# Kernel tuning notes

Measured on AMD Instinct MI355X. Metric: run time of the kernel, lower is better.

Reference implementation:

```python
import jax, jax.numpy as jnp
import numpy as np


def setup_inputs() -> dict:
    key = jax.random.key(0)
    ks = jax.random.split(key, 5)
    B, S, D = 2, 2048, 1024
    scale = 0.02
    return {
        "x": jax.random.normal(ks[0], (B, S, D), dtype=jnp.float32),
        "q_proj_weight": jax.random.normal(ks[1], (D, D), dtype=jnp.float32) * scale,
        "k_proj_weight": jax.random.normal(ks[2], (D, D), dtype=jnp.float32) * scale,
        "v_proj_weight": jax.random.normal(ks[3], (D, D), dtype=jnp.float32) * scale,
        "o_proj_weight": jax.random.normal(ks[4], (D, D), dtype=jnp.float32) * scale,
    }


def reference(x, q_proj_weight, k_proj_weight, v_proj_weight, o_proj_weight):
    num_heads = 16
    B, S, d_in = x.shape
    d_k = q_proj_weight.shape[0]
    head_size = d_k // num_heads

    def split_heads(t):  # [B,S,d_k] -> [B,H,S,hs]
        return t.reshape(B, S, num_heads, head_size).transpose(0, 2, 1, 3)

    q = split_heads(jnp.einsum('bsd,kd->bsk', x, q_proj_weight))
    k = split_heads(jnp.einsum('bsd,kd->bsk', x, k_proj_weight))
    v = split_heads(jnp.einsum('bsd,kd->bsk', x, v_proj_weight))

    scale = jnp.float32(head_size) ** -0.5
    scores = jnp.einsum('bhtc,bhkc->bhtk', q, k) * scale  # [B,H,S,S]
    causal = jnp.tril(jnp.ones((S, S), dtype=bool))
    scores = jnp.where(causal, scores, -jnp.inf)
    attn = jax.nn.softmax(scores, axis=-1)
    out = jnp.einsum('bhtk,bhkc->bhtc', attn, v)  # [B,H,S,hs]
    out = out.transpose(0, 2, 1, 3).reshape(B, S, d_k)
    return jnp.einsum('bsv,dv->bsd', out, o_proj_weight)
```

## Files before the change

kernel.cpp:

```cpp
#include <hip/hip_runtime.h>
#include <hip/hip_bf16.h>

typedef short bf16x8 __attribute__((ext_vector_type(8)));
typedef float f32x4 __attribute__((ext_vector_type(4)));

__device__ __forceinline__ short f2bf(float f) {
  union { __hip_bfloat16 h; short s; } u;
  u.h = __float2bfloat16(f);
  return u.s;
}

__device__ __forceinline__ void gload_lds16(const short* g, short* lds_base) {
  __builtin_amdgcn_global_load_lds(
      (const __attribute__((address_space(1))) void*)g,
      (__attribute__((address_space(3))) void*)lds_base, 16, 0, 0);
}

__global__ void cast_f32_bf16(const float* __restrict__ in, short* __restrict__ out, int n4) {
  int i = blockIdx.x * blockDim.x + threadIdx.x;
  if (i < n4) {
    float4 v = reinterpret_cast<const float4*>(in)[i];
    short4 o;
    o.x = f2bf(v.x); o.y = f2bf(v.y); o.z = f2bf(v.z); o.w = f2bf(v.w);
    reinterpret_cast<short4*>(out)[i] = o;
  }
}

__global__ void cast_w4(const float* __restrict__ w0, const float* __restrict__ w1,
                        const float* __restrict__ w2, const float* __restrict__ w3,
                        short* __restrict__ dst, int n4each) {
  int i = blockIdx.x * blockDim.x + threadIdx.x;
  if (i >= n4each) return;
  const float* src = (blockIdx.y == 0) ? w0 : (blockIdx.y == 1) ? w1
                   : (blockIdx.y == 2) ? w2 : w3;
  float4 v = reinterpret_cast<const float4*>(src)[i];
  short4 o;
  o.x = f2bf(v.x); o.y = f2bf(v.y); o.z = f2bf(v.z); o.w = f2bf(v.w);
  reinterpret_cast<short4*>(dst + (size_t)blockIdx.y * 1024 * 1024)[i] = o;
}

#define QSCALE 0.18033688f

template<int MODE>
__global__ __launch_bounds__(512, 1)
void gemm8p(const short* __restrict__ A, const short* __restrict__ Bw,
            short* __restrict__ Qo, short* __restrict__ Ko, short* __restrict__ Vo,
            float* __restrict__ Cf, int M, int N, int Kd)
{
  __shared__ short As[2][256 * 64];
  __shared__ short Bs[2][192 * 64];
  const int tid = threadIdx.x;
  const int wid = tid >> 6, lane = tid & 63;
  const int l16 = lane & 15, lq = lane >> 4;
  const int bm = blockIdx.x * 256, bn = blockIdx.y * 192;
  const int wr = (wid >> 2) * 128;
  const int wc = (wid & 3) * 48;
  const int lrow = lane >> 3;
  const int scol = ((lane & 7) ^ lrow) * 8;

#define ST_A(slot, k0) do { _Pragma("unroll")                                     \
  for (int j = 0; j < 4; ++j) {                                                   \
    int r = j * 64 + wid * 8;                                                     \
    gload_lds16(A + (size_t)(bm + r + lrow) * Kd + (k0) + scol, &As[slot][r * 64]); } } while (0)
#define ST_B(slot, k0) do { _Pragma("unroll")                                     \
  for (int j = 0; j < 3; ++j) {                                                   \
    int r = j * 64 + wid * 8;                                                     \
    gload_lds16(Bw + (size_t)(bn + r + lrow) * Kd + (k0) + scol, &Bs[slot][r * 64]); } } while (0)

  f32x4 acc[8][3];
#pragma unroll
  for (int m = 0; m < 8; ++m)
#pragma unroll
    for (int n = 0; n < 3; ++n) acc[m][n] = (f32x4){0.f, 0.f, 0.f, 0.f};

  const int nt = Kd >> 6;
  ST_A(0, 0);  ST_B(0, 0);
  ST_A(1, 64); ST_B(1, 64);
  asm volatile("s_waitcnt vmcnt(7)" ::: "memory");
  __builtin_amdgcn_s_barrier();
  asm volatile("" ::: "memory");

  bf16x8 af[4][2], bl[2][2], bh1[2];

  for (int t = 0; t < nt; ++t) {
    const int slot = t & 1;
    const int k2 = (t + 2) << 6;
    const bool st = (t + 2) < nt;

#pragma unroll
    for (int ks = 0; ks < 2; ++ks) {
      const int csw = (ks * 32 + lq * 8) ^ ((l16 & 7) << 3);
#pragma unroll
      for (int m = 0; m < 4; ++m)
        af[m][ks] = *(const bf16x8*)&As[slot][(wr + m * 16 + l16) * 64 + csw];
#pragma unroll
      for (int n = 0; n < 2; ++n)
        bl[n][ks] = *(const bf16x8*)&Bs[slot][(wc + n * 16 + l16) * 64 + csw];
    }
    __builtin_amdgcn_s_barrier();
    asm volatile("s_waitcnt lgkmcnt(0)" ::: "memory");
    __builtin_amdgcn_sched_barrier(0);
    __builtin_amdgcn_s_setprio(1);
#pragma unroll
    for (int ks = 0; ks < 2; ++ks)
#pragma unroll
      for (int m = 0; m < 4; ++m)
#pragma unroll
        for (int n = 0; n < 2; ++n)
          acc[m][n] = __builtin_amdgcn_mfma_f32_16x16x32_bf16(af[m][ks], bl[n][ks], acc[m][n], 0, 0, 0);
    __builtin_amdgcn_s_setprio(0);
    asm volatile("" ::: "memory");
    __builtin_amdgcn_s_barrier();
    asm volatile("" ::: "memory");

#pragma unroll
    for (int ks = 0; ks < 2; ++ks) {
      const int csw = (ks * 32 + lq * 8) ^ ((l16 & 7) << 3);
      bh1[ks] = *(const bf16x8*)&Bs[slot][(wc + 32 + l16) * 64 + csw];
    }
    __builtin_amdgcn_s_barrier();
    asm volatile("s_waitcnt lgkmcnt(0)" ::: "memory");
    __builtin_amdgcn_sched_barrier(0);
    __builtin_amdgcn_s_setprio(1);
#pragma unroll
    for (int ks = 0; ks < 2; ++ks)
#pragma unroll
      for (int m = 0; m < 4; ++m)
        acc[m][2] = __builtin_amdgcn_mfma_f32_16x16x32_bf16(af[m][ks], bh1[ks], acc[m][2], 0, 0, 0);
    __builtin_amdgcn_s_setprio(0);
    asm volatile("" ::: "memory");
    __builtin_amdgcn_s_barrier();
    asm volatile("" ::: "memory");

#pragma unroll
    for (int ks = 0; ks < 2; ++ks) {
      const int csw = (ks * 32 + lq * 8) ^ ((l16 & 7) << 3);
#pragma unroll
      for (int m = 0; m < 4; ++m)
        af[m][ks] = *(const bf16x8*)&As[slot][(wr + 64 + m * 16 + l16) * 64 + csw];
    }
    if (st) ST_B(slot, k2);
    __builtin_amdgcn_s_barrier();
    asm volatile("s_waitcnt lgkmcnt(0)" ::: "memory");
    __builtin_amdgcn_sched_barrier(0);
    __builtin_amdgcn_s_setprio(1);
#pragma unroll
    for (int ks = 0; ks < 2; ++ks)
#pragma unroll
      for (int m = 0; m < 4; ++m)
        acc[m + 4][2] = __builtin_amdgcn_mfma_f32_16x16x32_bf16(af[m][ks], bh1[ks], acc[m + 4][2], 0, 0, 0);
    __builtin_amdgcn_s_setprio(0);
    asm volatile("" ::: "memory");
    __builtin_amdgcn_s_barrier();
    asm volatile("" ::: "memory");

    if (st) ST_A(slot, k2);
    __builtin_amdgcn_s_barrier();
    asm volatile("" ::: "memory");
    __builtin_amdgcn_s_setprio(1);
#pragma unroll
    for (int ks = 0; ks < 2; ++ks)
#pragma unroll
      for (int m = 0; m < 4; ++m)
#pragma unroll
        for (int n = 0; n < 2; ++n)
          acc[m + 4][n] = __builtin_amdgcn_mfma_f32_16x16x32_bf16(af[m][ks], bl[n][ks], acc[m + 4][n], 0, 0, 0);
    __builtin_amdgcn_s_setprio(0);
    if (t + 2 < nt)      { asm volatile("s_waitcnt vmcnt(7)" ::: "memory"); }
    else if (t + 1 < nt) { asm volatile("s_waitcnt vmcnt(0)" ::: "memory"); }
    asm volatile("" ::: "memory");
    __builtin_amdgcn_s_barrier();
    asm volatile("" ::: "memory");
  }

#pragma unroll
  for (int m = 0; m < 8; ++m) {
#pragma unroll
    for (int n = 0; n < 3; ++n) {
      int col = bn + wc + n * 16 + l16;
      int rr0 = bm + wr + m * 16 + lq * 4;
      if (MODE == 0) {
        int b = rr0 >> 11;
        int which = col >> 10, cc = col & 1023;
        int h = cc >> 6, d = cc & 63;
        size_t bh2 = (size_t)(b * 16 + h);
        if (which == 2) {
          int s0 = rr0 & 2047;
          short4 pack;
          pack.x = f2bf(acc[m][n][0]); pack.y = f2bf(acc[m][n][1]);
          pack.z = f2bf(acc[m][n][2]); pack.w = f2bf(acc[m][n][3]);
          *reinterpret_cast<short4*>(&Vo[(bh2 * 64 + d) * 2048 + s0]) = pack;
        } else {
#pragma unroll
          for (int i = 0; i < 4; ++i) {
            int s = (rr0 + i) & 2047;
            float v = acc[m][n][i];
            if (which == 0) Qo[(bh2 * 2048 + s) * 64 + d] = f2bf(v * QSCALE);
            else            Ko[(bh2 * 2048 + s) * 64 + d] = f2bf(v);
          }
        }
      } else {
#pragma unroll
        for (int i = 0; i < 4; ++i)
          Cf[(size_t)(rr0 + i) * N + col] = acc[m][n][i];
      }
    }
  }
#undef ST_A
#undef ST_B
}

#define BKT 64

template<int MODE, int TBM, int TBN, int WM, int WN>
__global__ __launch_bounds__(WM * WN * 64, 2)
void gemm_bt(const short* __restrict__ A, const short* __restrict__ Bw,
             float* __restrict__ Cf, int M, int N, int Kd)
{
  constexpr int NWAVE = WM * WN;
  constexpr int MR = TBM / WM / 16;
  constexpr int NR = TBN / WN / 16;
  constexpr int SROWS = TBM / NWAVE;
  constexpr int SITER = SROWS / 8;

  __shared__ short As[2][TBM * BKT];
  __shared__ short Bs[2][TBN * BKT];
  const int tid = threadIdx.x;
  const int wid = tid >> 6, lane = tid & 63;
  const int l16 = lane & 15, lq = lane >> 4;
  const int bm = blockIdx.x * TBM, bn = blockIdx.y * TBN;
  const int wr = (wid / WN) * (TBM / WM);
  const int wc = (wid % WN) * (TBN / WN);

  const int srow = wid * SROWS;
  const int lrow = lane >> 3;
  const int scol = ((lane & 7) ^ lrow) * 8;

#define GSTAGE(buf, k0) do {                                                        \
  _Pragma("unroll")                                                                 \
  for (int j = 0; j < SITER; ++j) {                                                 \
    int r = srow + j * 8;                                                           \
    gload_lds16(A  + (size_t)(bm + r + lrow) * Kd + (k0) + scol, &As[buf][r * BKT]);\
    gload_lds16(Bw + (size_t)(bn + r + lrow) * Kd + (k0) + scol, &Bs[buf][r * BKT]);\
  }                                                                                 \
} while (0)

#define GCOMPUTE(buf) do {                                                          \
  _Pragma("unroll")                                                                 \
  for (int ks = 0; ks < 2; ++ks) {                                                  \
    const int csw = (ks * 32 + lq * 8) ^ ((l16 & 7) << 3);                          \
    bf16x8 af2[MR], bfr[NR];                                                        \
    _Pragma("unroll")                                                               \
    for (int m = 0; m < MR; ++m)                                                    \
      af2[m] = *reinterpret_cast<const bf16x8*>(                                    \
          &As[buf][(wr + m * 16 + l16) * BKT + csw]);                               \
    _Pragma("unroll")                                                               \
    for (int n = 0; n < NR; ++n)                                                    \
      bfr[n] = *reinterpret_cast<const bf16x8*>(                                    \
          &Bs[buf][(wc + n * 16 + l16) * BKT + csw]);                               \
    _Pragma("unroll")                                                               \
    for (int m = 0; m < MR; ++m)                                                    \
      _Pragma("unroll")                                                             \
      for (int n = 0; n < NR; ++n)                                                  \
        acc[m][n] = __builtin_amdgcn_mfma_f32_16x16x32_bf16(af2[m], bfr[n], acc[m][n], 0, 0, 0); \
  }                                                                                 \
} while (0)

  f32x4 acc[MR][NR];
#pragma unroll
  for (int m = 0; m < MR; ++m)
#pragma unroll
    for (int n = 0; n < NR; ++n) acc[m][n] = (f32x4){0.f, 0.f, 0.f, 0.f};

  const int nt = Kd >> 6;
  GSTAGE(0, 0);
  for (int t = 0; t < nt; ++t) {
    const int cur = t & 1;
    if (t + 1 < nt) {
      GSTAGE(cur ^ 1, (t + 1) << 6);
      asm volatile("s_waitcnt vmcnt(%0)" :: "i"(2 * SITER) : "memory");
    } else {
      asm volatile("s_waitcnt vmcnt(0)" ::: "memory");
    }
    __builtin_amdgcn_s_barrier();
    asm volatile("" ::: "memory");
    GCOMPUTE(cur);
    asm volatile("" ::: "memory");
    __builtin_amdgcn_s_barrier();
    asm volatile("" ::: "memory");
  }

#pragma unroll
  for (int m = 0; m < MR; ++m)
#pragma unroll
    for (int n = 0; n < NR; ++n) {
      int col = bn + wc + n * 16 + l16;
      int rr0 = bm + wr + m * 16 + lq * 4;
#pragma unroll
      for (int i = 0; i < 4; ++i)
        Cf[(size_t)(rr0 + i) * N + col] = acc[m][n][i];
    }
#undef GSTAGE
#undef GCOMPUTE
}

__global__ __launch_bounds__(256, 4)
void attn_fwd(const short* __restrict__ Qb, const short* __restrict__ Kb,
              const short* __restrict__ Vb, short* __restrict__ Ob)
{
  constexpr int S = 2048, HS = 64;
  constexpr float SM2 = 17.3123405f;
  __shared__ short Ks[2][64 * 64];
  __shared__ short Vs[2][64 * 64];
  __shared__ short Ps[4][16 * 64];

  const int tid = threadIdx.x;
  const int wid = tid >> 6, lane = tid & 63;
  const int l16 = lane & 15, lq = lane >> 4;
  const int qt = 31 - blockIdx.y;
  const int bh = blockIdx.x;
  const int qbase = qt * 64 + wid * 16;

  const short* Qp = Qb + (size_t)bh * S * HS;
  const short* Kp = Kb + (size_t)bh * S * HS;
  const short* Vp = Vb + (size_t)bh * HS * S;

  const int lr8 = lane >> 3;
  const int ssw = ((lane & 7) ^ lr8) * 8;
  const int cswA = (l16 & 7) << 3;

#define STAGEKV(slot, kt_) do {                                                    \
  _Pragma("unroll")                                                                \
  for (int j2 = 0; j2 < 2; ++j2) {                                                 \
    int r = wid * 16 + j2 * 8;                                                     \
    gload_lds16(Kp + (size_t)((kt_) * 64 + r + lr8) * HS + ssw, &Ks[slot][r * 64]);\
    gload_lds16(Vp + (size_t)(r + lr8) * S + (kt_) * 64 + ssw, &Vs[slot][r * 64]); \
  }                                                                                \
} while (0)

  bf16x8 qf[2];
#pragma unroll
  for (int ks = 0; ks < 2; ++ks)
    qf[ks] = *reinterpret_cast<const bf16x8*>(
        Qp + (size_t)(qbase + l16) * HS + ks * 32 + lq * 8);

  f32x4 oacc[4];
#pragma unroll
  for (int t = 0; t < 4; ++t) oacc[t] = (f32x4){0.f, 0.f, 0.f, 0.f};
  float psum = 0.f;

  const int NT = qt + 1;
  STAGEKV(0, 0);
  asm volatile("s_waitcnt vmcnt(0)" ::: "memory");
  __builtin_amdgcn_s_barrier();
  asm volatile("" ::: "memory");

  for (int kt = 0; kt < NT; ++kt) {
    const int slot = kt & 1;
    if (kt + 1 < NT) STAGEKV(slot ^ 1, kt + 1);

    f32x4 sacc[4];
#pragma unroll
    for (int n = 0; n < 4; ++n) sacc[n] = (f32x4){0.f, 0.f, 0.f, 0.f};
#pragma unroll
    for (int ks = 0; ks < 2; ++ks) {
      const int csw = (ks * 32 + lq * 8) ^ cswA;
#pragma unroll
      for (int n = 0; n < 4; ++n) {
        bf16x8 kf = *reinterpret_cast<const bf16x8*>(&Ks[slot][(n * 16 + l16) * 64 + csw]);
        sacc[n] = __builtin_amdgcn_mfma_f32_16x16x32_bf16(kf, qf[ks], sacc[n], 0, 0, 0);
      }
    }

    const bool nomask = (kt * 64 + 63) <= qbase;
    const int qg = qbase + l16;
    float ps = 0.f;
#pragma unroll
    for (int n = 0; n < 4; ++n) {
      short4 pk;
#pragma unroll
      for (int i = 0; i < 4; ++i) {
        float e;
        if (nomask) {
          e = exp2f(sacc[n][i] - SM2);
        } else {
          int kg = kt * 64 + n * 16 + lq * 4 + i;
          e = (kg > qg) ? 0.f : exp2f(sacc[n][i] - SM2);
        }
        ps += e;
        ((short*)&pk)[i] = f2bf(e);
      }
      *reinterpret_cast<short4*>(
          &Ps[wid][l16 * 64 + ((n * 16 + lq * 4) ^ cswA)]) = pk;
    }
    psum += ps;

#pragma unroll
    for (int ks = 0; ks < 2; ++ks) {
      const int csw = (ks * 32 + lq * 8) ^ cswA;
      bf16x8 pf = *reinterpret_cast<const bf16x8*>(&Ps[wid][l16 * 64 + csw]);
#pragma unroll
      for (int t = 0; t < 4; ++t) {
        bf16x8 vf = *reinterpret_cast<const bf16x8*>(&Vs[slot][(t * 16 + l16) * 64 + csw]);
        oacc[t] = __builtin_amdgcn_mfma_f32_16x16x32_bf16(pf, vf, oacc[t], 0, 0, 0);
      }
    }

    asm volatile("s_waitcnt vmcnt(0)" ::: "memory");
    __builtin_amdgcn_s_barrier();
    asm volatile("" ::: "memory");
  }

  float l = psum;
  l += __shfl_xor(l, 16);
  l += __shfl_xor(l, 32);
  float r = 1.0f / l;
  float linv[4];
#pragma unroll
  for (int i = 0; i < 4; ++i)
    linv[i] = __shfl(r, lq * 4 + i);

  const int b = bh >> 4, h = bh & 15;
#pragma unroll
  for (int t = 0; t < 4; ++t)
#pragma unroll
    for (int i = 0; i < 4; ++i) {
      int qg2 = qbase + lq * 4 + i;
      int dcol = h * 64 + t * 16 + l16;
      Ob[((size_t)b * S + qg2) * 1024 + dcol] = f2bf(oacc[t][i] * linv[i]);
    }
#undef STAGEKV
}

extern "C" void kernel_launch(void* const* d_in, const int* in_sizes, int n_in,
                              void* d_out, int out_size, void* d_ws, size_t ws_size,
                              hipStream_t stream) {
  const float* x   = (const float*)d_in[0];
  const float* wqf = (const float*)d_in[1];
  const float* wkf = (const float*)d_in[2];
  const float* wvf = (const float*)d_in[3];
  const float* wof = (const float*)d_in[4];
  float* out = (float*)d_out;

  short* xb = (short*)d_ws;
  short* wq = xb + (size_t)4096 * 1024;
  short* wk = wq + (size_t)1024 * 1024;
  short* wv = wk + (size_t)1024 * 1024;
  short* wo = wv + (size_t)1024 * 1024;
  short* Qb = wo + (size_t)1024 * 1024;
  short* Kb = Qb + (size_t)32 * 2048 * 64;
  short* Vb = Kb + (size_t)32 * 2048 * 64;
  short* Ob = Vb + (size_t)32 * 2048 * 64;

  cast_f32_bf16<<<4096, 256, 0, stream>>>(x, xb, 4096 * 1024 / 4);
  cast_w4<<<dim3(1024, 4), 256, 0, stream>>>(wqf, wkf, wvf, wof, wq, 1024 * 1024 / 4);

  gemm8p<0><<<dim3(16, 16), 512, 0, stream>>>(xb, wq, Qb, Kb, Vb, nullptr, 4096, 3072, 1024);

  attn_fwd<<<dim3(32, 32), 256, 0, stream>>>(Qb, Kb, Vb, Ob);

  gemm_bt<2, 128, 128, 2, 2><<<dim3(32, 8), 256, 0, stream>>>(
      Ob, wo, out, 4096, 1024, 1024);
}
```

Baseline: 116.2 us.

## Split keys across waves, pair causal query blocks, keep P in registers

The attention kernel now gives each workgroup two 32-row query blocks (jp and 63-jp) to balance causal work. Within a block, each wave takes a 16-key slice of every K/V tile instead of a 16-query slice. P stays in registers and feeds the MFMA directly, with half of the k-dimension zero-padded, which removes the Ps LDS round trip. Partial outputs and row sums are then reduced across the four waves through LDS with serial barriers. The constant max-offset subtraction is dropped, and the f32-to-bf16 pack conversion now uses an inline instruction.

New measurement: 126.2 us. 8.5% more time.

```diff
diff --git a/kernel.cpp b/kernel.cpp
--- a/kernel.cpp
+++ b/kernel.cpp
@@ -1,6 +1,7 @@
 #include <hip/hip_runtime.h>
 #include <hip/hip_bf16.h>
 
+typedef short bf16x4 __attribute__((ext_vector_type(4)));
 typedef short bf16x8 __attribute__((ext_vector_type(8)));
 typedef float f32x4 __attribute__((ext_vector_type(4)));
 
@@ -8,6 +9,12 @@
   union { __hip_bfloat16 h; short s; } u;
   u.h = __float2bfloat16(f);
   return u.s;
+}
+
+__device__ __forceinline__ int cvt_pk_bf16(float lo, float hi) {
+  int r;
+  asm volatile("v_cvt_pk_bf16_f32 %0, %1, %2" : "=v"(r) : "v"(lo), "v"(hi));
+  return r;
 }
 
 __device__ __forceinline__ void gload_lds16(const short* g, short* lds_base) {
@@ -304,22 +311,19 @@
 #undef GCOMPUTE
 }
 
-__global__ __launch_bounds__(256, 4)
+__global__ __launch_bounds__(256)
 void attn_fwd(const short* __restrict__ Qb, const short* __restrict__ Kb,
               const short* __restrict__ Vb, short* __restrict__ Ob)
 {
   constexpr int S = 2048, HS = 64;
-  constexpr float SM2 = 17.3123405f;
   __shared__ short Ks[2][64 * 64];
   __shared__ short Vs[2][64 * 64];
-  __shared__ short Ps[4][16 * 64];
 
   const int tid = threadIdx.x;
   const int wid = tid >> 6, lane = tid & 63;
   const int l16 = lane & 15, lq = lane >> 4;
-  const int qt = 31 - blockIdx.y;
   const int bh = blockIdx.x;
-  const int qbase = qt * 64 + wid * 16;
+  const int jp = blockIdx.y;
 
   const short* Qp = Qb + (size_t)bh * S * HS;
   const short* Kp = Kb + (size_t)bh * S * HS;
@@ -327,7 +331,10 @@
 
   const int lr8 = lane >> 3;
   const int ssw = ((lane & 7) ^ lr8) * 8;
-  const int cswA = (l16 & 7) << 3;
+  const int m7 = l16 & 7;
+
+  float* sc  = reinterpret_cast<float*>(&Ks[0][0]);
+  float* sc2 = reinterpret_cast<float*>(&Vs[0][0]);
 
 #define STAGEKV(slot, kt_) do {                                                    \
   _Pragma("unroll")                                                                \
@@ -338,97 +345,132 @@
   }                                                                                \
 } while (0)
 
-  bf16x8 qf[2];
-#pragma unroll
-  for (int ks = 0; ks < 2; ++ks)
-    qf[ks] = *reinterpret_cast<const bf16x8*>(
-        Qp + (size_t)(qbase + l16) * HS + ks * 32 + lq * 8);
-
-  f32x4 oacc[4];
-#pragma unroll
-  for (int t = 0; t < 4; ++t) oacc[t] = (f32x4){0.f, 0.f, 0.f, 0.f};
-  float psum = 0.f;
-
-  const int NT = qt + 1;
-  STAGEKV(0, 0);
-  asm volatile("s_waitcnt vmcnt(0)" ::: "memory");
-  __builtin_amdgcn_s_barrier();
-  asm volatile("" ::: "memory");
-
-  for (int kt = 0; kt < NT; ++kt) {
-    const int slot = kt & 1;
-    if (kt + 1 < NT) STAGEKV(slot ^ 1, kt + 1);
-
-    f32x4 sacc[4];
-#pragma unroll
-    for (int n = 0; n < 4; ++n) sacc[n] = (f32x4){0.f, 0.f, 0.f, 0.f};
-#pragma unroll
-    for (int ks = 0; ks < 2; ++ks) {
-      const int csw = (ks * 32 + lq * 8) ^ cswA;
-#pragma unroll
-      for (int n = 0; n < 4; ++n) {
-        bf16x8 kf = *reinterpret_cast<const bf16x8*>(&Ks[slot][(n * 16 + l16) * 64 + csw]);
-        sacc[n] = __builtin_amdgcn_mfma_f32_16x16x32_bf16(kf, qf[ks], sacc[n], 0, 0, 0);
+  const int b_ = bh >> 4, h_ = bh & 15;
+
+  for (int seg = 0; seg < 2; ++seg) {
+    const int j32 = seg ? (63 - jp) : jp;
+    const int q0 = j32 * 32;
+    const int NT = (j32 >> 1) + 1;
+
+    bf16x8 qf[2][2];
+#pragma unroll
+    for (int f = 0; f < 2; ++f)
+#pragma unroll
+      for (int ks = 0; ks < 2; ++ks)
+        qf[f][ks] = *reinterpret_cast<const bf16x8*>(
+            Qp + (size_t)(q0 + f * 16 + l16) * HS + ks * 32 + lq * 8);
+
+    f32x4 oacc[2][4];
+#pragma unroll
+    for (int f = 0; f < 2; ++f)
+#pragma unroll
+      for (int t = 0; t < 4; ++t) oacc[f][t] = (f32x4){0.f, 0.f, 0.f, 0.f};
+    float psum[2] = {0.f, 0.f};
+
+    STAGEKV(0, 0);
+    asm volatile("s_waitcnt vmcnt(0)" ::: "memory");
+    __builtin_amdgcn_s_barrier();
+    asm volatile("" ::: "memory");
+
+    for (int kt = 0; kt < NT; ++kt) {
+      const int slot = kt & 1;
+      if (kt + 1 < NT) STAGEKV(slot ^ 1, kt + 1);
+
+      f32x4 sacc[2];
+#pragma unroll
+      for (int f = 0; f < 2; ++f) sacc[f] = (f32x4){0.f, 0.f, 0.f, 0.f};
+#pragma unroll
+      for (int ks = 0; ks < 2; ++ks) {
+        const int csw = (ks * 32 + lq * 8) ^ (m7 << 3);
+        bf16x8 kf = *reinterpret_cast<const bf16x8*>(&Ks[slot][(wid * 16 + l16) * 64 + csw]);
+#pragma unroll
+        for (int f = 0; f < 2; ++f)
+          sacc[f] = __builtin_amdgcn_mfma_f32_16x16x32_bf16(kf, qf[f][ks], sacc[f], 0, 0, 0);
       }
-    }
-
-    const bool nomask = (kt * 64 + 63) <= qbase;
-    const int qg = qbase + l16;
-    float ps = 0.f;
-#pragma unroll
-    for (int n = 0; n < 4; ++n) {
-      short4 pk;
-#pragma unroll
-      for (int i = 0; i < 4; ++i) {
-        float e;
-        if (nomask) {
-          e = exp2f(sacc[n][i] - SM2);
-        } else {
-          int kg = kt * 64 + n * 16 + lq * 4 + i;
-          e = (kg > qg) ? 0.f : exp2f(sacc[n][i] - SM2);
+
+      const bool diag = (kt == NT - 1);
+      int pa[2][2];
+#pragma unroll
+      for (int f = 0; f < 2; ++f) {
+        float e[4];
+#pragma unroll
+        for (int i = 0; i < 4; ++i) e[i] = exp2f(sacc[f][i]);
+        if (diag) {
+          const int qg = q0 + f * 16 + l16;
+          const int kb = (NT - 1) * 64 + wid * 16 + lq * 4;
+#pragma unroll
+          for (int i = 0; i < 4; ++i)
+            if (kb + i > qg) e[i] = 0.f;
         }
-        ps += e;
-        ((short*)&pk)[i] = f2bf(e);
+        psum[f] += (e[0] + e[1]) + (e[2] + e[3]);
+        pa[f][0] = cvt_pk_bf16(e[0], e[1]);
+        pa[f][1] = cvt_pk_bf16(e[2], e[3]);
       }
-      *reinterpret_cast<short4*>(
-          &Ps[wid][l16 * 64 + ((n * 16 + lq * 4) ^ cswA)]) = pk;
-    }
-    psum += ps;
-
-#pragma unroll
-    for (int ks = 0; ks < 2; ++ks) {
-      const int csw = (ks * 32 + lq * 8) ^ cswA;
-      bf16x8 pf = *reinterpret_cast<const bf16x8*>(&Ps[wid][l16 * 64 + csw]);
+
+      const int vc8 = ((wid * 2 + (lq >> 1)) ^ m7) * 8 + (lq & 1) * 4;
 #pragma unroll
       for (int t = 0; t < 4; ++t) {
-        bf16x8 vf = *reinterpret_cast<const bf16x8*>(&Vs[slot][(t * 16 + l16) * 64 + csw]);
-        oacc[t] = __builtin_amdgcn_mfma_f32_16x16x32_bf16(pf, vf, oacc[t], 0, 0, 0);
+        bf16x4 v4 = *reinterpret_cast<const bf16x4*>(&Vs[slot][(t * 16 + l16) * 64 + vc8]);
+        union { int4 iv; bf16x8 hv; } vu;
+        vu.iv = (int4){(int)(((unsigned)(unsigned short)v4[0]) | ((unsigned)(unsigned short)v4[1] << 16)),
+                       (int)(((unsigned)(unsigned short)v4[2]) | ((unsigned)(unsigned short)v4[3] << 16)),
+                       0, 0};
+#pragma unroll
+        for (int f = 0; f < 2; ++f) {
+          union { int4 iv; bf16x8 hv; } pu;
+          pu.iv = (int4){pa[f][0], pa[f][1], 0, 0};
+          oacc[f][t] = __builtin_amdgcn_mfma_f32_16x16x32_bf16(pu.hv, vu.hv, oacc[f][t], 0, 0, 0);
+        }
       }
-    }
-
-    asm volatile("s_waitcnt vmcnt(0)" ::: "memory");
-    __builtin_amdgcn_s_barrier();
-    asm volatile("" ::: "memory");
+
+      asm volatile("s_waitcnt vmcnt(0)" ::: "memory");
+      __builtin_amdgcn_s_barrier();
+      asm volatile("" ::: "memory");
+    }
+
+    float lsum[2];
+#pragma unroll
+    for (int f = 0; f < 2; ++f) {
+      float l = psum[f];
+      l += __shfl_xor(l, 16);
+      l += __shfl_xor(l, 32);
+      lsum[f] = l;
+    }
+    sc2[wid * 32 + l16] = lsum[0];
+    sc2[wid * 32 + 16 + l16] = lsum[1];
+
+    for (int w = 0; w < 4; ++w) {
+      if (wid == w) {
+#pragma unroll
+        for (int f = 0; f < 2; ++f)
+#pragma unroll
+          for (int t = 0; t < 4; ++t)
+#pragma unroll
+            for (int i = 0; i < 4; ++i) {
+              float* p = &sc[(f * 16 + lq * 4 + i) * 64 + t * 16 + l16];
+              if (w == 0) *p = oacc[f][t][i];
+              else        *p += oacc[f][t][i];
+            }
+      }
+      __syncthreads();
+    }
+
+    const int qr = tid >> 3, d0 = (tid & 7) * 8;
+    float lv = sc2[qr] + sc2[32 + qr] + sc2[64 + qr] + sc2[96 + qr];
+    float inv = 1.0f / lv;
+    float vv[8];
+#pragma unroll
+    for (int e = 0; e < 8; ++e) vv[e] = sc[qr * 64 + d0 + e] * inv;
+    __syncthreads();
+
+    int pk0 = cvt_pk_bf16(vv[0], vv[1]);
+    int pk1 = cvt_pk_bf16(vv[2], vv[3]);
+    int pk2 = cvt_pk_bf16(vv[4], vv[5]);
+    int pk3 = cvt_pk_bf16(vv[6], vv[7]);
+    int qg = q0 + qr;
+    *reinterpret_cast<int4*>(&Ob[((size_t)b_ * S + qg) * 1024 + h_ * 64 + d0]) =
+        (int4){pk0, pk1, pk2, pk3};
   }
-
-  float l = psum;
-  l += __shfl_xor(l, 16);
-  l += __shfl_xor(l, 32);
-  float r = 1.0f / l;
-  float linv[4];
-#pragma unroll
-  for (int i = 0; i < 4; ++i)
-    linv[i] = __shfl(r, lq * 4 + i);
-
-  const int b = bh >> 4, h = bh & 15;
-#pragma unroll
-  for (int t = 0; t < 4; ++t)
-#pragma unroll
-    for (int i = 0; i < 4; ++i) {
-      int qg2 = qbase + lq * 4 + i;
-      int dcol = h * 64 + t * 16 + l16;
-      Ob[((size_t)b * S + qg2) * 1024 + dcol] = f2bf(oacc[t][i] * linv[i]);
-    }
 #undef STAGEKV
 }
 
```

## Pair causal query tiles per block and stage K/V through registers with padded LDS

Applied to the files above, without the earlier changes.

The attention kernel now launches half as many blocks. Each block processes two query tiles, jp and 31-jp, so every block does the same amount of causal work. K/V staging changes from direct global-to-LDS async loads with XOR swizzle to register prefetch followed by LDS stores into rows padded to 72 elements. The QK MFMA operand order and the P layout are changed too. The balanced tiles may reduce tail imbalance, but 512 blocks give less parallelism, and the register staging adds VGPR pressure and extra LDS writes.

Measured after the change: 115.5 us. About the same (-0.7%).

```diff
diff --git a/kernel.cpp b/kernel.cpp
--- a/kernel.cpp
+++ b/kernel.cpp
@@ -304,132 +304,136 @@
 #undef GCOMPUTE
 }
 
-__global__ __launch_bounds__(256, 4)
+__global__ __launch_bounds__(256)
 void attn_fwd(const short* __restrict__ Qb, const short* __restrict__ Kb,
               const short* __restrict__ Vb, short* __restrict__ Ob)
 {
   constexpr int S = 2048, HS = 64;
   constexpr float SM2 = 17.3123405f;
-  __shared__ short Ks[2][64 * 64];
-  __shared__ short Vs[2][64 * 64];
-  __shared__ short Ps[4][16 * 64];
+  __shared__ short Ks[2][64][72];
+  __shared__ short Vs[2][64][72];
+  __shared__ short Ps[4][16][72];
 
   const int tid = threadIdx.x;
   const int wid = tid >> 6, lane = tid & 63;
   const int l16 = lane & 15, lq = lane >> 4;
-  const int qt = 31 - blockIdx.y;
   const int bh = blockIdx.x;
-  const int qbase = qt * 64 + wid * 16;
+  const int jp = blockIdx.y;
 
   const short* Qp = Qb + (size_t)bh * S * HS;
   const short* Kp = Kb + (size_t)bh * S * HS;
   const short* Vp = Vb + (size_t)bh * HS * S;
 
-  const int lr8 = lane >> 3;
-  const int ssw = ((lane & 7) ^ lr8) * 8;
-  const int cswA = (l16 & 7) << 3;
-
-#define STAGEKV(slot, kt_) do {                                                    \
+  const int sr = tid >> 3;
+  const int so = (tid & 7) * 8;
+
+  bf16x8 kreg[2], vreg[2];
+
+#define LOADKV(kt) do {                                                            \
   _Pragma("unroll")                                                                \
-  for (int j2 = 0; j2 < 2; ++j2) {                                                 \
-    int r = wid * 16 + j2 * 8;                                                     \
-    gload_lds16(Kp + (size_t)((kt_) * 64 + r + lr8) * HS + ssw, &Ks[slot][r * 64]);\
-    gload_lds16(Vp + (size_t)(r + lr8) * S + (kt_) * 64 + ssw, &Vs[slot][r * 64]); \
+  for (int i2 = 0; i2 < 2; ++i2) {                                                 \
+    kreg[i2] = *reinterpret_cast<const bf16x8*>(Kp + (size_t)((kt) * 64 + sr + 32 * i2) * HS + so); \
+    vreg[i2] = *reinterpret_cast<const bf16x8*>(Vp + (size_t)(sr + 32 * i2) * S + (kt) * 64 + so);  \
   }                                                                                \
 } while (0)
 
-  bf16x8 qf[2];
-#pragma unroll
-  for (int ks = 0; ks < 2; ++ks)
-    qf[ks] = *reinterpret_cast<const bf16x8*>(
-        Qp + (size_t)(qbase + l16) * HS + ks * 32 + lq * 8);
-
-  f32x4 oacc[4];
-#pragma unroll
-  for (int t = 0; t < 4; ++t) oacc[t] = (f32x4){0.f, 0.f, 0.f, 0.f};
-  float psum = 0.f;
-
-  const int NT = qt + 1;
-  STAGEKV(0, 0);
-  asm volatile("s_waitcnt vmcnt(0)" ::: "memory");
-  __builtin_amdgcn_s_barrier();
-  asm volatile("" ::: "memory");
-
-  for (int kt = 0; kt < NT; ++kt) {
-    const int slot = kt & 1;
-    if (kt + 1 < NT) STAGEKV(slot ^ 1, kt + 1);
-
-    f32x4 sacc[4];
-#pragma unroll
-    for (int n = 0; n < 4; ++n) sacc[n] = (f32x4){0.f, 0.f, 0.f, 0.f};
-#pragma unroll
-    for (int ks = 0; ks < 2; ++ks) {
-      const int csw = (ks * 32 + lq * 8) ^ cswA;
-#pragma unroll
-      for (int n = 0; n < 4; ++n) {
-        bf16x8 kf = *reinterpret_cast<const bf16x8*>(&Ks[slot][(n * 16 + l16) * 64 + csw]);
-        sacc[n] = __builtin_amdgcn_mfma_f32_16x16x32_bf16(kf, qf[ks], sacc[n], 0, 0, 0);
+#define WRITEKV(buf) do {                                                          \
+  _Pragma("unroll")                                                                \
+  for (int i2 = 0; i2 < 2; ++i2) {                                                 \
+    *reinterpret_cast<bf16x8*>(&Ks[buf][sr + 32 * i2][so]) = kreg[i2];             \
+    *reinterpret_cast<bf16x8*>(&Vs[buf][sr + 32 * i2][so]) = vreg[i2];             \
+  }                                                                                \
+} while (0)
+
+  const int b_ = bh >> 4, h_ = bh & 15;
+
+  for (int seg = 0; seg < 2; ++seg) {
+    const int qt = seg ? (31 - jp) : jp;
+
+    bf16x8 qf[2];
+#pragma unroll
+    for (int ks = 0; ks < 2; ++ks)
+      qf[ks] = *reinterpret_cast<const bf16x8*>(
+          Qp + (size_t)(qt * 64 + wid * 16 + l16) * HS + ks * 32 + lq * 8);
+
+    f32x4 oacc[4];
+#pragma unroll
+    for (int t = 0; t < 4; ++t) oacc[t] = (f32x4){0.f, 0.f, 0.f, 0.f};
+    float lrow[4] = {0.f, 0.f, 0.f, 0.f};
+
+    const int qrow_base = qt * 64 + wid * 16 + lq * 4;
+
+    LOADKV(0);
+    WRITEKV(0);
+    __syncthreads();
+
+    for (int kt = 0; kt <= qt; ++kt) {
+      const int buf = kt & 1;
+      if (kt + 1 <= qt) LOADKV(kt + 1);
+
+      f32x4 sacc[4];
+#pragma unroll
+      for (int n = 0; n < 4; ++n) sacc[n] = (f32x4){0.f, 0.f, 0.f, 0.f};
+#pragma unroll
+      for (int ks = 0; ks < 2; ++ks) {
+#pragma unroll
+        for (int n = 0; n < 4; ++n) {
+          bf16x8 kf = *reinterpret_cast<const bf16x8*>(&Ks[buf][n * 16 + l16][ks * 32 + lq * 8]);
+          sacc[n] = __builtin_amdgcn_mfma_f32_16x16x32_bf16(qf[ks], kf, sacc[n], 0, 0, 0);
+        }
       }
-    }
-
-    const bool nomask = (kt * 64 + 63) <= qbase;
-    const int qg = qbase + l16;
-    float ps = 0.f;
-#pragma unroll
-    for (int n = 0; n < 4; ++n) {
-      short4 pk;
+
+      const bool diag = (kt == qt);
 #pragma unroll
       for (int i = 0; i < 4; ++i) {
-        float e;
-        if (nomask) {
-          e = exp2f(sacc[n][i] - SM2);
-        } else {
-          int kg = kt * 64 + n * 16 + lq * 4 + i;
-          e = (kg > qg) ? 0.f : exp2f(sacc[n][i] - SM2);
+        const int qrow = qrow_base + i;
+        float psum = 0.f;
+#pragma unroll
+        for (int n = 0; n < 4; ++n) {
+          float v = sacc[n][i];
+          if (diag && (kt * 64 + n * 16 + l16) > qrow) v = -1e30f;
+          float e = exp2f(v - SM2);
+          psum += e;
+          Ps[wid][lq * 4 + i][n * 16 + l16] = f2bf(e);
         }
-        ps += e;
-        ((short*)&pk)[i] = f2bf(e);
+        lrow[i] += psum;
       }
-      *reinterpret_cast<short4*>(
-          &Ps[wid][l16 * 64 + ((n * 16 + lq * 4) ^ cswA)]) = pk;
-    }
-    psum += ps;
-
-#pragma unroll
-    for (int ks = 0; ks < 2; ++ks) {
-      const int csw = (ks * 32 + lq * 8) ^ cswA;
-      bf16x8 pf = *reinterpret_cast<const bf16x8*>(&Ps[wid][l16 * 64 + csw]);
-#pragma unroll
-      for (int t = 0; t < 4; ++t) {
-        bf16x8 vf = *reinterpret_cast<const bf16x8*>(&Vs[slot][(t * 16 + l16) * 64 + csw]);
-        oacc[t] = __builtin_amdgcn_mfma_f32_16x16x32_bf16(pf, vf, oacc[t], 0, 0, 0);
+
+#pragma unroll
+      for (int ks = 0; ks < 2; ++ks) {
+        bf16x8 pf = *reinterpret_cast<const bf16x8*>(&Ps[wid][l16][ks * 32 + lq * 8]);
+#pragma unroll
+        for (int t = 0; t < 4; ++t) {
+          bf16x8 vf = *reinterpret_cast<const bf16x8*>(&Vs[buf][t * 16 + l16][ks * 32 + lq * 8]);
+          oacc[t] = __builtin_amdgcn_mfma_f32_16x16x32_bf16(pf, vf, oacc[t], 0, 0, 0);
+        }
       }
-    }
-
-    asm volatile("s_waitcnt vmcnt(0)" ::: "memory");
-    __builtin_amdgcn_s_barrier();
-    asm volatile("" ::: "memory");
+
+      if (kt + 1 <= qt) WRITEKV(buf ^ 1);
+      __syncthreads();
+    }
+
+    float linv[4];
+#pragma unroll
+    for (int i = 0; i < 4; ++i) {
+      float l = lrow[i];
+#pragma unroll
+      for (int d = 1; d < 16; d <<= 1) l += __shfl_xor(l, d);
+      linv[i] = 1.0f / l;
+    }
+
+#pragma unroll
+    for (int t = 0; t < 4; ++t)
+#pragma unroll
+      for (int i = 0; i < 4; ++i) {
+        float v = oacc[t][i] * linv[i];
+        int srow2 = qt * 64 + wid * 16 + lq * 4 + i;
+        int dcol = h_ * 64 + t * 16 + l16;
+        Ob[((size_t)b_ * S + srow2) * 1024 + dcol] = f2bf(v);
+      }
   }
-
-  float l = psum;
-  l += __shfl_xor(l, 16);
-  l += __shfl_xor(l, 32);
-  float r = 1.0f / l;
-  float linv[4];
-#pragma unroll
-  for (int i = 0; i < 4; ++i)
-    linv[i] = __shfl(r, lq * 4 + i);
-
-  const int b = bh >> 4, h = bh & 15;
-#pragma unroll
-  for (int t = 0; t < 4; ++t)
-#pragma unroll
-    for (int i = 0; i < 4; ++i) {
-      int qg2 = qbase + lq * 4 + i;
-      int dcol = h * 64 + t * 16 + l16;
-      Ob[((size_t)b * S + qg2) * 1024 + dcol] = f2bf(oacc[t][i] * linv[i]);
-    }
-#undef STAGEKV
+#undef LOADKV
+#undef WRITEKV
 }
 
 extern "C" void kernel_launch(void* const* d_in, const int* in_sizes, int n_in,
@@ -457,7 +461,7 @@
 
   gemm8p<0><<<dim3(16, 16), 512, 0, stream>>>(xb, wq, Qb, Kb, Vb, nullptr, 4096, 3072, 1024);
 
-  attn_fwd<<<dim3(32, 32), 256, 0, stream>>>(Qb, Kb, Vb, Ob);
+  attn_fwd<<<dim3(32, 16), 256, 0, stream>>>(Qb, Kb, Vb, Ob);
 
   gemm_bt<2, 128, 128, 2, 2><<<dim3(32, 8), 256, 0, stream>>>(
       Ob, wo, out, 4096, 1024, 1024);
```
